# Optimization experiments

Measured on AMD Instinct MI355X. Metric: run time of the kernel, lower is better.

Reference implementation:

```python
import jax, jax.numpy as jnp
import numpy as np
import math

N_HEAD = 16
ROPE_BASE = 10000.0


def _rope_cos_sin(seq_len, head_dim, dtype):
    # standard RoPE tables: freqs_i = base^(-2i/d), i in [0, d/2)
    half = head_dim // 2
    inv_freq = ROPE_BASE ** (-(jnp.arange(half, dtype=jnp.float32) * 2.0 / head_dim))
    t = jnp.arange(seq_len, dtype=jnp.float32)
    ang = t[:, None] * inv_freq[None, :]  # [S, d/2]
    return jnp.cos(ang).astype(dtype), jnp.sin(ang).astype(dtype)


def _apply_rope(x, cos, sin):
    # x: [B, S, H, d]; rotate interleaved even/odd pairs
    x1 = x[..., 0::2]
    x2 = x[..., 1::2]
    c = cos[None, :, None, :]
    s = sin[None, :, None, :]
    out = jnp.stack([x1 * c - x2 * s, x1 * s + x2 * c], axis=-1)
    return out.reshape(x.shape)


def setup_inputs() -> dict:
    key = jax.random.key(0)
    kx, kq, kk, kv, ko = jax.random.split(key, 5)
    B, S, H = 2, 2048, 1024
    x = jax.random.normal(kx, (B, S, H), dtype=jnp.float32)
    scale = 0.02
    w_q = jax.random.normal(kq, (H, H), dtype=jnp.float32) * scale
    w_k = jax.random.normal(kk, (H, H), dtype=jnp.float32) * scale
    w_v = jax.random.normal(kv, (H, H), dtype=jnp.float32) * scale
    w_o = jax.random.normal(ko, (H, H), dtype=jnp.float32) * scale
    return {"x": x, "w_q": w_q, "w_k": w_k, "w_v": w_v, "w_o": w_o}


def reference(x, w_q, w_k, w_v, w_o):
    B, S, H = x.shape
    d = H // N_HEAD
    # torch nn.Linear(bias=False): y = x @ W^T, W is [out, in]
    q = (x @ w_q.T).reshape(B, S, N_HEAD, d)
    k = (x @ w_k.T).reshape(B, S, N_HEAD, d)
    v = (x @ w_v.T).reshape(B, S, N_HEAD, d)
    cos, sin = _rope_cos_sin(S, d, x.dtype)
    q = _apply_rope(q, cos, sin)
    k = _apply_rope(k, cos, sin)
    scores = jnp.einsum("bqhd,bkhd->bhqk", q, k) / math.sqrt(d)
    coefs = jax.nn.softmax(scores, axis=-1)
    # NOTE: causal mask is applied AFTER softmax via tril (no renormalization)
    causal = jnp.tril(jnp.ones((S, S), dtype=bool))
    coefs = jnp.where(causal[None, None], coefs, 0.0)
    out = jnp.einsum("bhqk,bkhd->bqhd", coefs, v).reshape(B, S, H)
    return out @ w_o.T
```

## Files before the change

kernel.cpp:

```cpp
#include <hip/hip_runtime.h>
#include <math.h>

#define SEQ   2048
#define HDIM  1024
#define NH    16
#define DH    64
#define MTOT  4096
#define BHTOT 32

typedef _Float16 half_t;
typedef __attribute__((ext_vector_type(2))) __fp16 fp16x2;
typedef __attribute__((ext_vector_type(4))) _Float16 half4;
typedef __attribute__((ext_vector_type(8))) _Float16 half8;
typedef __attribute__((ext_vector_type(4))) float float4v;

typedef __attribute__((address_space(1))) const unsigned int guint;
typedef __attribute__((address_space(3))) unsigned int luint;
__device__ __forceinline__ void glds16(const half_t* g, half_t* l) {
    __builtin_amdgcn_global_load_lds((guint*)g, (luint*)l, 16, 0, 0);
}

__global__ __launch_bounds__(256)
void prep(const float* __restrict__ x,  const float* __restrict__ wq,
          const float* __restrict__ wk, const float* __restrict__ wv,
          const float* __restrict__ wo,
          half_t* __restrict__ xh,  half_t* __restrict__ wqh,
          half_t* __restrict__ wkh, half_t* __restrict__ wvh,
          half_t* __restrict__ woh, float2* __restrict__ rope)
{
    const int bid = blockIdx.x;
    if (bid < 8192) {
        int i = bid * 256 + threadIdx.x;
        const float* s; half_t* d;
        if (i < 1048576) { s = x; d = xh; }
        else {
            int j = i - 1048576;
            int w = j >> 18; i = j & 262143;
            s = (w == 0) ? wq : (w == 1) ? wk : (w == 2) ? wv : wo;
            d = (w == 0) ? wqh : (w == 1) ? wkh : (w == 2) ? wvh : woh;
        }
        float4 v = ((const float4*)s)[i];
        union { half_t h[4]; uint2 u; } tmp;
        tmp.h[0] = (half_t)v.x; tmp.h[1] = (half_t)v.y;
        tmp.h[2] = (half_t)v.z; tmp.h[3] = (half_t)v.w;
        ((uint2*)d)[i] = tmp.u;
    } else {
        int tt = (bid - 8192) * 256 + threadIdx.x;
        int s = tt >> 5, j = tt & 31;
        float inv = powf(10000.0f, -(float)j / 32.0f);
        float ang = (float)s * inv;
        rope[tt] = make_float2(cosf(ang), sinf(ang));
    }
}

__global__ __launch_bounds__(256)
void gemm_qkv(const half_t* __restrict__ A,
              const half_t* __restrict__ w0, const half_t* __restrict__ w1,
              const half_t* __restrict__ w2,
              half_t* __restrict__ Qb, half_t* __restrict__ Kb,
              half_t* __restrict__ Vtb, float* __restrict__ outF,
              const float2* __restrict__ rope, int mode_base)
{
    const int mode = mode_base + blockIdx.z;
    const half_t* Bw = (mode == 1) ? w1 : (mode == 2) ? w2 : w0;

    __shared__ __align__(16) half_t Ash[128][32];
    __shared__ __align__(16) half_t Bsh[128][32];

    const int t    = threadIdx.x;
    const int lane = t & 63;
    const int wave = t >> 6;
    const int quad = lane >> 4;
    const int l16  = lane & 15;
    const int wr   = (wave >> 1) * 64;
    const int wc   = (wave & 1) * 64;
    const int bm   = blockIdx.x, bn = blockIdx.y;

    const int srow = lane >> 2, spos = lane & 3;
    const half_t* Asrc0 = A  + (size_t)(bm * 128 + wave * 32      + srow) * HDIM + spos * 8;
    const half_t* Asrc1 = A  + (size_t)(bm * 128 + wave * 32 + 16 + srow) * HDIM + spos * 8;
    const half_t* Bsrc0 = Bw + (size_t)(bn * 128 + wave * 32      + srow) * HDIM + spos * 8;
    const half_t* Bsrc1 = Bw + (size_t)(bn * 128 + wave * 32 + 16 + srow) * HDIM + spos * 8;
    half_t* Adst0 = &Ash[wave * 32][0];
    half_t* Adst1 = &Ash[wave * 32 + 16][0];
    half_t* Bdst0 = &Bsh[wave * 32][0];
    half_t* Bdst1 = &Bsh[wave * 32 + 16][0];

    float4v acc[4][4] = {};

    for (int kt = 0; kt < HDIM / 32; ++kt) {
        glds16(Asrc0, Adst0);
        glds16(Asrc1, Adst1);
        glds16(Bsrc0, Bdst0);
        glds16(Bsrc1, Bdst1);
        Asrc0 += 32; Asrc1 += 32; Bsrc0 += 32; Bsrc1 += 32;
        __syncthreads();
        half8 af[4], bf[4];
#pragma unroll
        for (int mb = 0; mb < 4; ++mb) af[mb] = *(const half8*)&Ash[wr + mb * 16 + l16][quad * 8];
#pragma unroll
        for (int nb = 0; nb < 4; ++nb) bf[nb] = *(const half8*)&Bsh[wc + nb * 16 + l16][quad * 8];
#pragma unroll
        for (int mb = 0; mb < 4; ++mb)
#pragma unroll
            for (int nb = 0; nb < 4; ++nb)
                acc[mb][nb] = __builtin_amdgcn_mfma_f32_16x16x32_f16(af[mb], bf[nb], acc[mb][nb], 0, 0, 0);
        __syncthreads();
    }

    if (mode == 3) {
#pragma unroll
        for (int mb = 0; mb < 4; ++mb)
#pragma unroll
            for (int nb = 0; nb < 4; ++nb) {
                int row0 = bm * 128 + wr + mb * 16 + quad * 4;
                int col  = bn * 128 + wc + nb * 16 + l16;
#pragma unroll
                for (int r = 0; r < 4; ++r)
                    outF[(size_t)(row0 + r) * HDIM + col] = acc[mb][nb][r];
            }
        return;
    }
    if (mode == 2) {
#pragma unroll
        for (int mb = 0; mb < 4; ++mb)
#pragma unroll
            for (int nb = 0; nb < 4; ++nb) {
                int row0 = bm * 128 + wr + mb * 16 + quad * 4;
                int col  = bn * 128 + wc + nb * 16 + l16;
                int b = row0 >> 11, s0 = row0 & 2047;
                int h = col >> 6,  dd = col & 63;
                union { half_t h4[4]; uint2 u; } tmp;
#pragma unroll
                for (int r = 0; r < 4; ++r) tmp.h4[r] = (half_t)acc[mb][nb][r];
                *(uint2*)&Vtb[((size_t)((b * NH + h) * DH + dd)) * SEQ + s0] = tmp.u;
            }
        return;
    }
    {
        half_t* Ob = (mode == 0) ? Qb : Kb;
        const float scl = (mode == 0) ? 0.125f * 1.44269504088896f : 1.0f;
#pragma unroll
        for (int mb = 0; mb < 4; ++mb)
#pragma unroll
            for (int nb = 0; nb < 4; ++nb) {
                int row0 = bm * 128 + wr + mb * 16 + quad * 4;
                int col  = bn * 128 + wc + nb * 16 + l16;
                int b = row0 >> 11;
                int h = col >> 6, dd = col & 63, j = dd >> 1;
#pragma unroll
                for (int r = 0; r < 4; ++r) {
                    float v  = acc[mb][nb][r];
                    float vp = __shfl_xor(v, 1, 64);
                    int s = (row0 + r) & 2047;
                    float2 cs = rope[s * 32 + j];
                    float res = ((col & 1) == 0) ? (v * cs.x - vp * cs.y)
                                                 : (vp * cs.y + v * cs.x);
                    Ob[((size_t)((b * NH + h) * SEQ + s)) * DH + dd] = (half_t)(res * scl);
                }
            }
    }
}

__global__ __launch_bounds__(256)
void attn_fused(const half_t* __restrict__ Qb, const half_t* __restrict__ Kb,
                const half_t* __restrict__ Vtb, half_t* __restrict__ AOut)
{
    const int qt = blockIdx.x;
    const int bh = blockIdx.y;

    __shared__ __align__(16) half_t Ksh[2][64][64];
    __shared__ __align__(16) half_t Vsh[2][64][72];

    const int t = threadIdx.x;
    const int wave = t >> 6, lane = t & 63, quad = lane >> 4, l16 = lane & 15;

    const int qs = qt * 64 + wave * 16 + l16;
    const half_t* Qp = Qb + ((size_t)bh * SEQ + qs) * DH + quad * 8;
    half8 qf0 = *(const half8*)Qp;
    half8 qf1 = *(const half8*)(Qp + 32);

    float4v o[4] = {};
    float lsum = 0.f;

    const int krow = lane >> 3, kpos = lane & 7;
    const int kchunk = kpos ^ krow;
    const half_t* Ksrc0 = Kb + ((size_t)bh * SEQ + wave * 16     + krow) * DH + kchunk * 8;
    const half_t* Ksrc1 = Kb + ((size_t)bh * SEQ + wave * 16 + 8 + krow) * DH + kchunk * 8;
    const int ko1 = ((quad ^ (l16 & 7)) * 8);
    const int ko2 = ko1 ^ 32;

    const int sr  = t >> 2;
    const int scc = (t & 3) * 16;
    const half_t* Vg = Vtb + ((size_t)bh * DH + sr) * SEQ + scc;

    glds16(Ksrc0, &Ksh[0][wave * 16][0]);
    glds16(Ksrc1, &Ksh[0][wave * 16 + 8][0]);
    *(uint4*)&Vsh[0][sr][scc]     = *(const uint4*)(Vg);
    *(uint4*)&Vsh[0][sr][scc + 8] = *(const uint4*)(Vg + 8);
    __syncthreads();

    for (int kt = 0; kt < SEQ / 64; ++kt) {
        const int cur = kt & 1, nxt = cur ^ 1;
        const bool have_next = (kt + 1 < SEQ / 64);
        const bool next_v    = (kt + 1 <= qt);

        uint4 va, vb;
        if (have_next) {
            const half_t* Kn = Ksrc0 + (size_t)(kt + 1) * 64 * DH;
            glds16(Kn,            &Ksh[nxt][wave * 16][0]);
            glds16(Kn + 8 * DH,   &Ksh[nxt][wave * 16 + 8][0]);
            if (next_v) {
                const half_t* Vgk = Vg + (kt + 1) * 64;
                va = *(const uint4*)(Vgk);
                vb = *(const uint4*)(Vgk + 8);
            }
        }

        float4v sc[4];
#pragma unroll
        for (int nb = 0; nb < 4; ++nb) {
            const half_t* kp = &Ksh[cur][nb * 16 + l16][0];
            half8 kf0 = *(const half8*)(kp + ko1);
            half8 kf1 = *(const half8*)(kp + ko2);
            float4v a = {};
            a = __builtin_amdgcn_mfma_f32_16x16x32_f16(kf0, qf0, a, 0, 0, 0);
            a = __builtin_amdgcn_mfma_f32_16x16x32_f16(kf1, qf1, a, 0, 0, 0);
            sc[nb] = a;
        }

#pragma unroll
        for (int nb = 0; nb < 4; ++nb)
#pragma unroll
            for (int r = 0; r < 4; ++r) {
                float e = __builtin_amdgcn_exp2f(sc[nb][r]);
                sc[nb][r] = e;
                lsum += e;
            }

        if (kt <= qt) {
            if (kt == qt) {
#pragma unroll
                for (int nb = 0; nb < 4; ++nb)
#pragma unroll
                    for (int r = 0; r < 4; ++r)
                        if (nb * 16 + quad * 4 + r > wave * 16 + l16) sc[nb][r] = 0.f;
            }
            half4 pf[4];
#pragma unroll
            for (int nb = 0; nb < 4; ++nb) {
                union { fp16x2 v2[2]; half4 v4; } u;
                u.v2[0] = __builtin_amdgcn_cvt_pkrtz(sc[nb][0], sc[nb][1]);
                u.v2[1] = __builtin_amdgcn_cvt_pkrtz(sc[nb][2], sc[nb][3]);
                pf[nb] = u.v4;
            }
#pragma unroll
            for (int md = 0; md < 4; ++md)
#pragma unroll
                for (int nb = 0; nb < 4; ++nb) {
                    half4 vf = *(const half4*)&Vsh[cur][md * 16 + l16][nb * 16 + quad * 4];
                    o[md] = __builtin_amdgcn_mfma_f32_16x16x16f16(vf, pf[nb], o[md], 0, 0, 0);
                }
        }

        if (have_next && next_v) {
            *(uint4*)&Vsh[nxt][sr][scc]     = va;
            *(uint4*)&Vsh[nxt][sr][scc + 8] = vb;
        }
        __syncthreads();
    }

    lsum += __shfl_xor(lsum, 16, 64);
    lsum += __shfl_xor(lsum, 32, 64);
    const float inv = 1.0f / lsum;

    half_t (*Osh)[72] = (half_t(*)[72]) & Vsh[0][wave * 16][0];
#pragma unroll
    for (int md = 0; md < 4; ++md)
#pragma unroll
        for (int r = 0; r < 4; ++r)
            Osh[l16][md * 16 + quad * 4 + r] = (half_t)(o[md][r] * inv);
    __asm__ volatile("s_waitcnt lgkmcnt(0)" ::: "memory");

    const int orow = lane >> 2, occ = (lane & 3) * 16;
    uint4 o0 = *(const uint4*)&Osh[orow][occ];
    uint4 o1 = *(const uint4*)&Osh[orow][occ + 8];
    const int b = bh >> 4, h = bh & 15;
    const int s = qt * 64 + wave * 16 + orow;
    half_t* dst = AOut + ((size_t)(b * SEQ + s)) * HDIM + h * DH + occ;
    *(uint4*)dst       = o0;
    *(uint4*)(dst + 8) = o1;
}

extern "C" void kernel_launch(void* const* d_in, const int* in_sizes, int n_in,
                              void* d_out, int out_size, void* d_ws, size_t ws_size,
                              hipStream_t stream)
{
    const float* x  = (const float*)d_in[0];
    const float* wq = (const float*)d_in[1];
    const float* wk = (const float*)d_in[2];
    const float* wv = (const float*)d_in[3];
    const float* wo = (const float*)d_in[4];
    float* out = (float*)d_out;

    char* ws = (char*)d_ws;
    size_t off = 0;
    auto alloc = [&](size_t bytes) -> void* {
        void* p = ws + off;
        off += (bytes + 255) & ~(size_t)255;
        return p;
    };
    half_t* xh   = (half_t*)alloc((size_t)MTOT * HDIM * 2);
    half_t* wqh  = (half_t*)alloc((size_t)HDIM * HDIM * 2);
    half_t* wkh  = (half_t*)alloc((size_t)HDIM * HDIM * 2);
    half_t* wvh  = (half_t*)alloc((size_t)HDIM * HDIM * 2);
    half_t* woh  = (half_t*)alloc((size_t)HDIM * HDIM * 2);
    half_t* Qb   = (half_t*)alloc((size_t)BHTOT * SEQ * DH * 2);
    half_t* Kb   = (half_t*)alloc((size_t)BHTOT * SEQ * DH * 2);
    half_t* Vtb  = (half_t*)alloc((size_t)BHTOT * SEQ * DH * 2);
    half_t* ah   = (half_t*)alloc((size_t)MTOT * HDIM * 2);
    float2* rope = (float2*)alloc((size_t)SEQ * 32 * sizeof(float2));

    prep<<<8448, 256, 0, stream>>>(x, wq, wk, wv, wo, xh, wqh, wkh, wvh, woh, rope);

    gemm_qkv<<<dim3(32, 8, 3), 256, 0, stream>>>(xh, wqh, wkh, wvh,
                                                 Qb, Kb, Vtb, nullptr, rope, 0);
    attn_fused<<<dim3(32, 32), 256, 0, stream>>>(Qb, Kb, Vtb, ah);
    gemm_qkv<<<dim3(32, 8, 1), 256, 0, stream>>>(ah, woh, woh, woh,
                                                 nullptr, nullptr, nullptr, out, rope, 3);
}
```

Baseline: 210.0 us.

## Process two 16-row query groups per wave in attention kernel

Each wave now handles 32 query rows (two 16-row groups) instead of 16, so each block covers 128 queries and the grid halves. Every K tile in shared memory and every V fragment load is reused for two sets of MFMAs, which halves K/V global traffic and LDS reads per query. The cost is more registers per thread, fewer blocks (512), and coarser causal granularity: the PV work is skipped per wave on a 32-row boundary, while QK and exp still run over all key tiles.

```diff
diff --git a/kernel.cpp b/kernel.cpp
--- a/kernel.cpp
+++ b/kernel.cpp
@@ -174,14 +174,18 @@
 
     const int t = threadIdx.x;
     const int wave = t >> 6, lane = t & 63, quad = lane >> 4, l16 = lane & 15;
-
-    const int qs = qt * 64 + wave * 16 + l16;
-    const half_t* Qp = Qb + ((size_t)bh * SEQ + qs) * DH + quad * 8;
-    half8 qf0 = *(const half8*)Qp;
-    half8 qf1 = *(const half8*)(Qp + 32);
-
-    float4v o[4] = {};
-    float lsum = 0.f;
+    const int q0 = qt * 128 + wave * 32;
+
+    half8 qf[2][2];
+#pragma unroll
+    for (int g = 0; g < 2; ++g) {
+        const half_t* Qp = Qb + ((size_t)bh * SEQ + q0 + g * 16 + l16) * DH + quad * 8;
+        qf[g][0] = *(const half8*)Qp;
+        qf[g][1] = *(const half8*)(Qp + 32);
+    }
+
+    float4v o[2][4] = {};
+    float lsum[2] = {0.f, 0.f};
 
     const int krow = lane >> 3, kpos = lane & 7;
     const int kchunk = kpos ^ krow;
@@ -200,16 +204,17 @@
     *(uint4*)&Vsh[0][sr][scc + 8] = *(const uint4*)(Vg + 8);
     __syncthreads();
 
+    const int qmax = qt * 128 + 127;
     for (int kt = 0; kt < SEQ / 64; ++kt) {
         const int cur = kt & 1, nxt = cur ^ 1;
         const bool have_next = (kt + 1 < SEQ / 64);
-        const bool next_v    = (kt + 1 <= qt);
+        const bool next_v    = ((kt + 1) * 64 <= qmax);
 
         uint4 va, vb;
         if (have_next) {
             const half_t* Kn = Ksrc0 + (size_t)(kt + 1) * 64 * DH;
-            glds16(Kn,            &Ksh[nxt][wave * 16][0]);
-            glds16(Kn + 8 * DH,   &Ksh[nxt][wave * 16 + 8][0]);
+            glds16(Kn,          &Ksh[nxt][wave * 16][0]);
+            glds16(Kn + 8 * DH, &Ksh[nxt][wave * 16 + 8][0]);
             if (next_v) {
                 const half_t* Vgk = Vg + (kt + 1) * 64;
                 va = *(const uint4*)(Vgk);
@@ -217,49 +222,62 @@
             }
         }
 
-        float4v sc[4];
+        float4v sc[2][4];
 #pragma unroll
         for (int nb = 0; nb < 4; ++nb) {
             const half_t* kp = &Ksh[cur][nb * 16 + l16][0];
             half8 kf0 = *(const half8*)(kp + ko1);
             half8 kf1 = *(const half8*)(kp + ko2);
-            float4v a = {};
-            a = __builtin_amdgcn_mfma_f32_16x16x32_f16(kf0, qf0, a, 0, 0, 0);
-            a = __builtin_amdgcn_mfma_f32_16x16x32_f16(kf1, qf1, a, 0, 0, 0);
-            sc[nb] = a;
-        }
-
-#pragma unroll
-        for (int nb = 0; nb < 4; ++nb)
-#pragma unroll
-            for (int r = 0; r < 4; ++r) {
-                float e = __builtin_amdgcn_exp2f(sc[nb][r]);
-                sc[nb][r] = e;
-                lsum += e;
-            }
-
-        if (kt <= qt) {
-            if (kt == qt) {
-#pragma unroll
-                for (int nb = 0; nb < 4; ++nb)
-#pragma unroll
-                    for (int r = 0; r < 4; ++r)
-                        if (nb * 16 + quad * 4 + r > wave * 16 + l16) sc[nb][r] = 0.f;
-            }
-            half4 pf[4];
-#pragma unroll
-            for (int nb = 0; nb < 4; ++nb) {
-                union { fp16x2 v2[2]; half4 v4; } u;
-                u.v2[0] = __builtin_amdgcn_cvt_pkrtz(sc[nb][0], sc[nb][1]);
-                u.v2[1] = __builtin_amdgcn_cvt_pkrtz(sc[nb][2], sc[nb][3]);
-                pf[nb] = u.v4;
-            }
+#pragma unroll
+            for (int g = 0; g < 2; ++g) {
+                float4v a = {};
+                a = __builtin_amdgcn_mfma_f32_16x16x32_f16(kf0, qf[g][0], a, 0, 0, 0);
+                a = __builtin_amdgcn_mfma_f32_16x16x32_f16(kf1, qf[g][1], a, 0, 0, 0);
+                sc[g][nb] = a;
+            }
+        }
+
+#pragma unroll
+        for (int g = 0; g < 2; ++g)
+#pragma unroll
+            for (int nb = 0; nb < 4; ++nb)
+#pragma unroll
+                for (int r = 0; r < 4; ++r) {
+                    float e = __builtin_amdgcn_exp2f(sc[g][nb][r]);
+                    sc[g][nb][r] = e;
+                    lsum[g] += e;
+                }
+
+        const int kbase = kt * 64;
+        if (kbase <= q0 + 31) {
+            if (kbase + 63 > q0) {
+#pragma unroll
+                for (int g = 0; g < 2; ++g) {
+                    int qg = q0 + g * 16 + l16;
+#pragma unroll
+                    for (int nb = 0; nb < 4; ++nb)
+#pragma unroll
+                        for (int r = 0; r < 4; ++r)
+                            if (kbase + nb * 16 + quad * 4 + r > qg) sc[g][nb][r] = 0.f;
+                }
+            }
+            half4 pf[2][4];
+#pragma unroll
+            for (int g = 0; g < 2; ++g)
+#pragma unroll
+                for (int nb = 0; nb < 4; ++nb) {
+                    union { fp16x2 v2[2]; half4 v4; } u;
+                    u.v2[0] = __builtin_amdgcn_cvt_pkrtz(sc[g][nb][0], sc[g][nb][1]);
+                    u.v2[1] = __builtin_amdgcn_cvt_pkrtz(sc[g][nb][2], sc[g][nb][3]);
+                    pf[g][nb] = u.v4;
+                }
 #pragma unroll
             for (int md = 0; md < 4; ++md)
 #pragma unroll
                 for (int nb = 0; nb < 4; ++nb) {
                     half4 vf = *(const half4*)&Vsh[cur][md * 16 + l16][nb * 16 + quad * 4];
-                    o[md] = __builtin_amdgcn_mfma_f32_16x16x16f16(vf, pf[nb], o[md], 0, 0, 0);
+                    o[0][md] = __builtin_amdgcn_mfma_f32_16x16x16f16(vf, pf[0][nb], o[0][md], 0, 0, 0);
+                    o[1][md] = __builtin_amdgcn_mfma_f32_16x16x16f16(vf, pf[1][nb], o[1][md], 0, 0, 0);
                 }
         }
 
@@ -270,26 +288,28 @@
         __syncthreads();
     }
 
-    lsum += __shfl_xor(lsum, 16, 64);
-    lsum += __shfl_xor(lsum, 32, 64);
-    const float inv = 1.0f / lsum;
-
-    half_t (*Osh)[72] = (half_t(*)[72]) & Vsh[0][wave * 16][0];
-#pragma unroll
-    for (int md = 0; md < 4; ++md)
-#pragma unroll
-        for (int r = 0; r < 4; ++r)
-            Osh[l16][md * 16 + quad * 4 + r] = (half_t)(o[md][r] * inv);
-    __asm__ volatile("s_waitcnt lgkmcnt(0)" ::: "memory");
-
+    const int b = bh >> 4, h = bh & 15;
     const int orow = lane >> 2, occ = (lane & 3) * 16;
-    uint4 o0 = *(const uint4*)&Osh[orow][occ];
-    uint4 o1 = *(const uint4*)&Osh[orow][occ + 8];
-    const int b = bh >> 4, h = bh & 15;
-    const int s = qt * 64 + wave * 16 + orow;
-    half_t* dst = AOut + ((size_t)(b * SEQ + s)) * HDIM + h * DH + occ;
-    *(uint4*)dst       = o0;
-    *(uint4*)(dst + 8) = o1;
+#pragma unroll
+    for (int g = 0; g < 2; ++g) {
+        float rs = lsum[g];
+        rs += __shfl_xor(rs, 16, 64);
+        rs += __shfl_xor(rs, 32, 64);
+        const float inv = 1.0f / rs;
+        half_t (*Osh)[72] = (half_t(*)[72]) & Vsh[g][wave * 16][0];
+#pragma unroll
+        for (int md = 0; md < 4; ++md)
+#pragma unroll
+            for (int r = 0; r < 4; ++r)
+                Osh[l16][md * 16 + quad * 4 + r] = (half_t)(o[g][md][r] * inv);
+        __asm__ volatile("s_waitcnt lgkmcnt(0)" ::: "memory");
+        uint4 o0 = *(const uint4*)&Osh[orow][occ];
+        uint4 o1 = *(const uint4*)&Osh[orow][occ + 8];
+        const int s = qt * 128 + wave * 32 + g * 16 + orow;
+        half_t* dst = AOut + ((size_t)(b * SEQ + s)) * HDIM + h * DH + occ;
+        *(uint4*)dst       = o0;
+        *(uint4*)(dst + 8) = o1;
+    }
 }
 
 extern "C" void kernel_launch(void* const* d_in, const int* in_sizes, int n_in,
@@ -325,7 +345,7 @@
 
     gemm_qkv<<<dim3(32, 8, 3), 256, 0, stream>>>(xh, wqh, wkh, wvh,
                                                  Qb, Kb, Vtb, nullptr, rope, 0);
-    attn_fused<<<dim3(32, 32), 256, 0, stream>>>(Qb, Kb, Vtb, ah);
+    attn_fused<<<dim3(16, 32), 256, 0, stream>>>(Qb, Kb, Vtb, ah);
     gemm_qkv<<<dim3(32, 8, 1), 256, 0, stream>>>(ah, woh, woh, woh,
                                                  nullptr, nullptr, nullptr, out, rope, 3);
 }
```

Result: no change. 207.2 us (-1.3%).
